# Optimization experiments

Measured on AMD Instinct MI355X. Metric: run time of the kernel, lower is better.

## Reference

```python
import jax, jax.numpy as jnp
import numpy as np

_NUM_RBF = 8
_R_MAX = 3.0  # randn point clouds have radius ~ sqrt(3)
_CENTERS = jnp.linspace(0.0, _R_MAX, _NUM_RBF)
_C15 = float(np.sqrt(15.0))
_C5 = float(np.sqrt(5.0))


def _sph_basis(positions):
    """map_3d_feats_to_basis_functions: 8x0e (radial RBFs) + 1x1o (l=1 SH) + 1x2e (l=2 SH)."""
    centered = positions - jnp.mean(positions, axis=-2, keepdims=True)  # [B,N,3]
    r = jnp.sqrt(jnp.sum(centered * centered, axis=-1) + 1e-12)         # [B,N]
    d = centered / r[..., None]                                         # unit directions
    x, y, z = d[..., 0], d[..., 1], d[..., 2]
    s0 = jnp.exp(-(r[..., None] - _CENTERS) ** 2)                       # [B,N,8] scalar feats (0e)
    sh1 = d                                                             # [B,N,3] (1o)
    sh2 = jnp.stack([_C15 * x * y,
                     _C15 * y * z,
                     0.5 * _C5 * (3.0 * z * z - 1.0),
                     _C15 * x * z,
                     0.5 * _C15 * (x * x - y * y)], axis=-1)            # [B,N,5] (2e)
    return s0, sh1, sh2


def _mix(feat, W):
    # Equivariant per-l channel mixing: feat [B, mul_in, dim_l], W [mul_in, mul_out]
    return jnp.einsum('bci,co->boi', feat, W) / jnp.sqrt(jnp.asarray(W.shape[0], feat.dtype))


def reference(positions, W1a, W1b, W1c, W1d, W2a, W2b, W2c):
    s0, sh1, sh2 = _sph_basis(positions)
    # avg_irreps_with_same_id: average over the N points axis
    s = jnp.mean(s0, axis=-2)[..., None]          # [B,8,1]  8x0e
    v = jnp.mean(sh1, axis=-2)[:, None, :]        # [B,1,3]  1x1o
    # (mean of sh2 is dropped: linear1 output has no 2e)
    # linear1: '8x0e+1x1o+1x2e' -> '6x0e+4x1o' -> '6x0e+4x1o'
    s = _mix(_mix(s, W1a), W1b)                   # [B,6,1]
    v = _mix(_mix(v, W1c), W1d)                   # [B,4,3]
    # linear2: '6x0e+4x1o' -> '6x0e+4x1o' -> '6x0e'
    s = _mix(_mix(s, W2a), W2b)                   # [B,6,1]
    _ = _mix(v, W2c)                              # mid 1o channel, dropped by '6x0e' output
    # torch.cat of the six 0e irreps -> [B,6]
    return s[..., 0]


def setup_inputs() -> dict:
    key = jax.random.key(0)
    ks = jax.random.split(key, 8)
    return {
        'positions': jax.random.normal(ks[0], (32768, 128, 3), dtype=jnp.float32),
        'W1a': jax.random.normal(ks[1], (8, 6), dtype=jnp.float32),
        'W1b': jax.random.normal(ks[2], (6, 6), dtype=jnp.float32),
        'W1c': jax.random.normal(ks[3], (1, 4), dtype=jnp.float32),
        'W1d': jax.random.normal(ks[4], (4, 4), dtype=jnp.float32),
        'W2a': jax.random.normal(ks[5], (6, 6), dtype=jnp.float32),
        'W2b': jax.random.normal(ks[6], (6, 6), dtype=jnp.float32),
        'W2c': jax.random.normal(ks[7], (4, 4), dtype=jnp.float32),
    }
```

## Files before the change

### kernel.cpp

```cpp
#include <hip/hip_runtime.h>


__global__ __launch_bounds__(256) void sph_fused(
    const float* __restrict__ pos,
    const float* __restrict__ W1a, const float* __restrict__ W1b,
    const float* __restrict__ W2a, const float* __restrict__ W2b,
    float* __restrict__ out, int nBatch)
{
    __shared__ float BB[36];
    __shared__ float CC[36];
    __shared__ float MM[64];

    const int t = threadIdx.x;

    if (t < 36) {
        const int c = t / 6, o = t - 6 * c;
        float s = 0.f;
        #pragma unroll
        for (int j = 0; j < 6; ++j) s += W2a[c * 6 + j] * W2b[j * 6 + o];
        BB[t] = s;
    }
    __syncthreads();
    if (t < 36) {
        const int c = t / 6, o = t - 6 * c;
        float s = 0.f;
        #pragma unroll
        for (int j = 0; j < 6; ++j) s += W1b[c * 6 + j] * BB[j * 6 + o];
        CC[t] = s;
    }
    __syncthreads();
    if (t < 64) {
        if (t < 48) {
            const int k = t / 6, o = t - 6 * k;
            float s = 0.f;
            #pragma unroll
            for (int c = 0; c < 6; ++c) s += W1a[k * 6 + c] * CC[c * 6 + o];
            MM[t] = s * (0.024056261216234408f / 128.0f);
        } else {
            MM[t] = 0.f;
        }
    }
    __syncthreads();

    const int lane = t & 63;
    const int wv   = t >> 6;
    const int lsub = lane & 7;
    const int batch = (blockIdx.x * 4 + wv) * 8 + (lane >> 3);
    if (batch >= nBatch) return;

    union { float4 q[12]; float s[48]; } u;
    const float4* p4 = reinterpret_cast<const float4*>(
        pos + (size_t)batch * 384 + lsub * 48);
    #pragma unroll
    for (int j = 0; j < 12; ++j) u.q[j] = p4[j];

    float sx = 0.f, sy = 0.f, sz = 0.f;
    #pragma unroll
    for (int i = 0; i < 16; ++i) {
        sx += u.s[3 * i + 0]; sy += u.s[3 * i + 1]; sz += u.s[3 * i + 2];
    }
    sx += __shfl_xor(sx, 1, 64); sy += __shfl_xor(sy, 1, 64); sz += __shfl_xor(sz, 1, 64);
    sx += __shfl_xor(sx, 2, 64); sy += __shfl_xor(sy, 2, 64); sz += __shfl_xor(sz, 2, 64);
    sx += __shfl_xor(sx, 4, 64); sy += __shfl_xor(sy, 4, 64); sz += __shfl_xor(sz, 4, 64);
    const float mx = sx * (1.f / 128.f), my = sy * (1.f / 128.f), mz = sz * (1.f / 128.f);

    float acc[8] = {0.f, 0.f, 0.f, 0.f, 0.f, 0.f, 0.f, 0.f};
    #pragma unroll
    for (int i = 0; i < 16; ++i) {
        const float dx = u.s[3 * i + 0] - mx;
        const float dy = u.s[3 * i + 1] - my;
        const float dz = u.s[3 * i + 2] - mz;
        const float r = sqrtf(dx * dx + dy * dy + dz * dz + 1e-12f);
        #pragma unroll
        for (int k = 0; k < 8; ++k) {
            const float d = r - (float)k * (3.0f / 7.0f);
            acc[k] += __expf(-(d * d));
        }
    }

    const int l0 = lsub & 1, l1 = (lsub >> 1) & 1, l2 = (lsub >> 2) & 1;
    float bj[4];
    #pragma unroll
    for (int j = 0; j < 4; ++j) {
        const float send = l0 ? acc[2 * j]     : acc[2 * j + 1];
        const float keep = l0 ? acc[2 * j + 1] : acc[2 * j];
        bj[j] = keep + __shfl_xor(send, 1, 64);
    }
    float cj[2];
    #pragma unroll
    for (int j = 0; j < 2; ++j) {
        const float send = l1 ? bj[2 * j]     : bj[2 * j + 1];
        const float keep = l1 ? bj[2 * j + 1] : bj[2 * j];
        cj[j] = keep + __shfl_xor(send, 2, 64);
    }
    float S;
    {
        const float send = l2 ? cj[0] : cj[1];
        const float keep = l2 ? cj[1] : cj[0];
        S = keep + __shfl_xor(send, 4, 64);
    }

    const int laneBase = lane & 56;
    float oacc = 0.f;
    #pragma unroll
    for (int k = 0; k < 8; ++k) {
        const float sk = __shfl(S, laneBase + k, 64);
        oacc += sk * MM[k * 6 + lsub];
    }
    if (lsub < 6) out[batch * 6 + lsub] = oacc;
}

extern "C" void kernel_launch(void* const* d_in, const int* in_sizes, int n_in,
                              void* d_out, int out_size, void* d_ws, size_t ws_size,
                              hipStream_t stream) {
    const float* pos = (const float*)d_in[0];
    const float* W1a = (const float*)d_in[1];
    const float* W1b = (const float*)d_in[2];
    const float* W2a = (const float*)d_in[5];
    const float* W2b = (const float*)d_in[6];
    float* out = (float*)d_out;

    const int nBatch = in_sizes[0] / 384;
    const int batchesPerBlock = 32;
    const int grid = (nBatch + batchesPerBlock - 1) / batchesPerBlock;

    sph_fused<<<dim3(grid), dim3(256), 0, stream>>>(pos, W1a, W1b, W2a, W2b, out, nBatch);
}
```

Before: 18.23 us.

## Stage coalesced loads through LDS, use 16 lanes per batch, factor RBF exponentials

Each wave now loads positions as fully coalesced float4 chunks and transposes them through a swizzled LDS staging buffer, so every lane handles 8 points and a 16-lane group covers one batch. The eight RBF exponentials per point are replaced by two exps plus a running product with precomputed constant weights. Output stores are gathered into 24 contiguous lanes, and each block now covers 16 batches instead of 32. This adds 24KB of LDS per block, which may limit occupancy. The stage writes and reads happen without a barrier, relying only on an lgkmcnt wait within the wave.

```diff
diff --git a/kernel.cpp b/kernel.cpp
--- a/kernel.cpp
+++ b/kernel.cpp
@@ -10,6 +10,7 @@
     __shared__ float BB[36];
     __shared__ float CC[36];
     __shared__ float MM[64];
+    __shared__ float4 stage[4][384];
 
     const int t = threadIdx.x;
 
@@ -42,42 +43,69 @@
     }
     __syncthreads();
 
+    const int w    = t >> 6;
     const int lane = t & 63;
-    const int wv   = t >> 6;
-    const int lsub = lane & 7;
-    const int batch = (blockIdx.x * 4 + wv) * 8 + (lane >> 3);
-    if (batch >= nBatch) return;
+    const int wave = blockIdx.x * 4 + w;
+    const int wbatch = wave * 4;
+    if (wbatch >= nBatch) return;
 
-    union { float4 q[12]; float s[48]; } u;
-    const float4* p4 = reinterpret_cast<const float4*>(
-        pos + (size_t)batch * 384 + lsub * 48);
+    const int nChunks = nBatch * 96;
+    const int wchunk  = wave * 384;
+    const float4* p4 = reinterpret_cast<const float4*>(pos);
     #pragma unroll
-    for (int j = 0; j < 12; ++j) u.q[j] = p4[j];
+    for (int j = 0; j < 6; ++j) {
+        const int q = j * 64 + lane;
+        int gc = wchunk + q;
+        if (gc >= nChunks) gc = nChunks - 1;
+        const float4 v = p4[gc];
+        const int o = (q * 171) >> 10;
+        const int s = q - 6 * o;
+        stage[w][s * 64 + (o ^ s)] = v;
+    }
+    asm volatile("s_waitcnt lgkmcnt(0)" ::: "memory");
+
+    union { float4 q4[6]; float f[24]; } u;
+    #pragma unroll
+    for (int s = 0; s < 6; ++s) u.q4[s] = stage[w][s * 64 + (lane ^ s)];
 
     float sx = 0.f, sy = 0.f, sz = 0.f;
     #pragma unroll
-    for (int i = 0; i < 16; ++i) {
-        sx += u.s[3 * i + 0]; sy += u.s[3 * i + 1]; sz += u.s[3 * i + 2];
+    for (int i = 0; i < 8; ++i) {
+        sx += u.f[3 * i + 0]; sy += u.f[3 * i + 1]; sz += u.f[3 * i + 2];
     }
-    sx += __shfl_xor(sx, 1, 64); sy += __shfl_xor(sy, 1, 64); sz += __shfl_xor(sz, 1, 64);
-    sx += __shfl_xor(sx, 2, 64); sy += __shfl_xor(sy, 2, 64); sz += __shfl_xor(sz, 2, 64);
-    sx += __shfl_xor(sx, 4, 64); sy += __shfl_xor(sy, 4, 64); sz += __shfl_xor(sz, 4, 64);
+    #pragma unroll
+    for (int m = 1; m <= 8; m <<= 1) {
+        sx += __shfl_xor(sx, m, 64);
+        sy += __shfl_xor(sy, m, 64);
+        sz += __shfl_xor(sz, m, 64);
+    }
     const float mx = sx * (1.f / 128.f), my = sy * (1.f / 128.f), mz = sz * (1.f / 128.f);
 
+    const float WK1 = 0.83220583f, WK2 = 0.47965235f, WK3 = 0.19146295f,
+                WK4 = 0.05293049f, WK5 = 0.01013418f, WK6 = 0.00134381f,
+                WK7 = 1.2340980e-4f;
     float acc[8] = {0.f, 0.f, 0.f, 0.f, 0.f, 0.f, 0.f, 0.f};
     #pragma unroll
-    for (int i = 0; i < 16; ++i) {
-        const float dx = u.s[3 * i + 0] - mx;
-        const float dy = u.s[3 * i + 1] - my;
-        const float dz = u.s[3 * i + 2] - mz;
-        const float r = sqrtf(dx * dx + dy * dy + dz * dz + 1e-12f);
-        #pragma unroll
-        for (int k = 0; k < 8; ++k) {
-            const float d = r - (float)k * (3.0f / 7.0f);
-            acc[k] += __expf(-(d * d));
-        }
+    for (int i = 0; i < 8; ++i) {
+        const float dx = u.f[3 * i + 0] - mx;
+        const float dy = u.f[3 * i + 1] - my;
+        const float dz = u.f[3 * i + 2] - mz;
+        const float r2 = fmaf(dx, dx, fmaf(dy, dy, fmaf(dz, dz, 1e-12f)));
+        const float r  = sqrtf(r2);
+        const float E0 = __expf(-r2);
+        const float Bf = __expf(r * (6.0f / 7.0f));
+        float p = E0;
+        acc[0] += E0;
+        p *= Bf; acc[1] = fmaf(p, WK1, acc[1]);
+        p *= Bf; acc[2] = fmaf(p, WK2, acc[2]);
+        p *= Bf; acc[3] = fmaf(p, WK3, acc[3]);
+        p *= Bf; acc[4] = fmaf(p, WK4, acc[4]);
+        p *= Bf; acc[5] = fmaf(p, WK5, acc[5]);
+        p *= Bf; acc[6] = fmaf(p, WK6, acc[6]);
+        p *= Bf; acc[7] = fmaf(p, WK7, acc[7]);
     }
 
+    const int lsub = lane & 15;
     const int l0 = lsub & 1, l1 = (lsub >> 1) & 1, l2 = (lsub >> 2) & 1;
     float bj[4];
     #pragma unroll
@@ -99,15 +127,18 @@
         const float keep = l2 ? cj[1] : cj[0];
         S = keep + __shfl_xor(send, 4, 64);
     }
+    S += __shfl_xor(S, 8, 64);
 
-    const int laneBase = lane & 56;
+    const int gb = lane & 48;
     float oacc = 0.f;
     #pragma unroll
-    for (int k = 0; k < 8; ++k) {
-        const float sk = __shfl(S, laneBase + k, 64);
-        oacc += sk * MM[k * 6 + lsub];
-    }
-    if (lsub < 6) out[batch * 6 + lsub] = oacc;
+    for (int k = 0; k < 8; ++k)
+        oacc = fmaf(__shfl(S, gb + k, 64), MM[k * 6 + lsub], oacc);
+
+    const int LL = (lane < 24) ? lane : 0;
+    const int g = LL / 6, r = LL - 6 * g;
+    const float val = __shfl(oacc, g * 16 + r, 64);
+    if (lane < 24 && (wbatch + g) < nBatch) out[wbatch * 6 + lane] = val;
 }
 
 extern "C" void kernel_launch(void* const* d_in, const int* in_sizes, int n_in,
@@ -121,7 +152,7 @@
     float* out = (float*)d_out;
 
     const int nBatch = in_sizes[0] / 384;
-    const int batchesPerBlock = 32;
+    const int batchesPerBlock = 16;
     const int grid = (nBatch + batchesPerBlock - 1) / batchesPerBlock;
 
     sph_fused<<<dim3(grid), dim3(256), 0, stream>>>(pos, W1a, W1b, W2a, W2b, out, nBatch);
```

New measurement: 17.42 us. 4.4% less time.

## Persistent double-buffered waves with DPP reductions and factored RBF exponentials

Applied to the files above, without the earlier changes.

Changes the kernel to a persistent grid capped at 1024 blocks, where each wave processes 4 batches per tile with 16 lanes per batch and software double-buffers the next tile's loads while computing the current one. Shuffle-based reductions become DPP row-rotate reductions across 16 lanes. The eight per-point RBF exponentials are replaced by two exps and a running product with precomputed weights, using exp(-(r-c_k)^2) = exp(-r^2)·exp(2rc_k)·exp(-c_k^2). This reduces transcendental work and hides memory latency, but the running-product factorisation may lose accuracy for large r.

```diff
diff --git a/kernel.cpp b/kernel.cpp
--- a/kernel.cpp
+++ b/kernel.cpp
@@ -1,15 +1,28 @@
 #include <hip/hip_runtime.h>
 
 
-__global__ __launch_bounds__(256) void sph_fused(
+template <int N>
+__device__ __forceinline__ float ror16(float v) {
+    return __int_as_float(__builtin_amdgcn_update_dpp(
+        0, __float_as_int(v), 0x120 | N, 0xF, 0xF, true));
+}
+__device__ __forceinline__ float rowsum16(float v) {
+    v += ror16<1>(v);
+    v += ror16<2>(v);
+    v += ror16<4>(v);
+    v += ror16<8>(v);
+    return v;
+}
+
+__global__ __launch_bounds__(256, 4) void sph_fused(
     const float* __restrict__ pos,
     const float* __restrict__ W1a, const float* __restrict__ W1b,
     const float* __restrict__ W2a, const float* __restrict__ W2b,
     float* __restrict__ out, int nBatch)
 {
-    __shared__ float BB[36];
-    __shared__ float CC[36];
-    __shared__ float MM[64];
+    __shared__ float BBs[36];
+    __shared__ float CCs[36];
+    __shared__ float MMs[48];
 
     const int t = threadIdx.x;
 
@@ -18,96 +31,126 @@
         float s = 0.f;
         #pragma unroll
         for (int j = 0; j < 6; ++j) s += W2a[c * 6 + j] * W2b[j * 6 + o];
-        BB[t] = s;
+        BBs[t] = s;
     }
     __syncthreads();
     if (t < 36) {
         const int c = t / 6, o = t - 6 * c;
         float s = 0.f;
         #pragma unroll
-        for (int j = 0; j < 6; ++j) s += W1b[c * 6 + j] * BB[j * 6 + o];
-        CC[t] = s;
+        for (int j = 0; j < 6; ++j) s += W1b[c * 6 + j] * BBs[j * 6 + o];
+        CCs[t] = s;
     }
     __syncthreads();
-    if (t < 64) {
-        if (t < 48) {
-            const int k = t / 6, o = t - 6 * k;
-            float s = 0.f;
-            #pragma unroll
-            for (int c = 0; c < 6; ++c) s += W1a[k * 6 + c] * CC[c * 6 + o];
-            MM[t] = s * (0.024056261216234408f / 128.0f);
-        } else {
-            MM[t] = 0.f;
-        }
+    if (t < 48) {
+        const int k = t / 6, o = t - 6 * k;
+        float s = 0.f;
+        #pragma unroll
+        for (int c = 0; c < 6; ++c) s += W1a[k * 6 + c] * CCs[c * 6 + o];
+        MMs[t] = s * (0.024056261216234408f / 128.0f);
     }
     __syncthreads();
 
     const int lane = t & 63;
-    const int wv   = t >> 6;
-    const int lsub = lane & 7;
-    const int batch = (blockIdx.x * 4 + wv) * 8 + (lane >> 3);
-    if (batch >= nBatch) return;
+    const int w    = t >> 6;
+    const int lsub = lane & 15;
+    const int grp  = lane >> 4;
 
-    union { float4 q[12]; float s[48]; } u;
-    const float4* p4 = reinterpret_cast<const float4*>(
-        pos + (size_t)batch * 384 + lsub * 48);
+    const int col = (lsub < 6) ? lsub : 0;
+    float Mcol[8];
     #pragma unroll
-    for (int j = 0; j < 12; ++j) u.q[j] = p4[j];
+    for (int k = 0; k < 8; ++k) Mcol[k] = MMs[k * 6 + col];
 
-    float sx = 0.f, sy = 0.f, sz = 0.f;
-    #pragma unroll
-    for (int i = 0; i < 16; ++i) {
-        sx += u.s[3 * i + 0]; sy += u.s[3 * i + 1]; sz += u.s[3 * i + 2];
+    const int nTiles = (nBatch + 3) >> 2;
+    const int nWaves = gridDim.x * 4;
+    int tile = blockIdx.x * 4 + w;
+    if (tile >= nTiles) return;
+
+    const float4* __restrict__ p4 = reinterpret_cast<const float4*>(pos);
+    const int maxC = nBatch * 96 - 6;
+
+    union Pts { float4 q[6]; float f[24]; };
+    Pts A, B;
+
+    const float WK1 = 0.83220583f, WK2 = 0.47965235f, WK3 = 0.19146295f,
+                WK4 = 0.05293049f, WK5 = 0.01013418f, WK6 = 0.00134381f,
+                WK7 = 1.2340980e-4f;
+
+#define LOADT(U, T) do {                                                   \
+    int base_ = (T) * 384 + grp * 96 + lsub * 6;                           \
+    if (base_ > maxC) base_ = maxC;    \
+    _Pragma("unroll")                                                      \
+    for (int j_ = 0; j_ < 6; ++j_) (U).q[j_] = p4[base_ + j_];             \
+} while (0)
+
+#define COMPUTE(U, T) do {                                                 \
+    float sx_ = 0.f, sy_ = 0.f, sz_ = 0.f;                                 \
+    _Pragma("unroll")                                                      \
+    for (int i_ = 0; i_ < 8; ++i_) {                                       \
+        sx_ += (U).f[3 * i_ + 0];                                          \
+        sy_ += (U).f[3 * i_ + 1];                                          \
+        sz_ += (U).f[3 * i_ + 2];                                          \
+    }                                                                      \
+    sx_ = rowsum16(sx_); sy_ = rowsum16(sy_); sz_ = rowsum16(sz_);         \
+    const float mx_ = sx_ * (1.f / 128.f);                                 \
+    const float my_ = sy_ * (1.f / 128.f);                                 \
+    const float mz_ = sz_ * (1.f / 128.f);                                 \
+    float a0_=0.f,a1_=0.f,a2_=0.f,a3_=0.f,a4_=0.f,a5_=0.f,a6_=0.f,a7_=0.f; \
+    _Pragma("unroll")                                                      \
+    for (int i_ = 0; i_ < 8; ++i_) {                                       \
+        const float dx_ = (U).f[3 * i_ + 0] - mx_;                         \
+        const float dy_ = (U).f[3 * i_ + 1] - my_;                         \
+        const float dz_ = (U).f[3 * i_ + 2] - mz_;                         \
+        const float r2_ = fmaf(dx_, dx_, fmaf(dy_, dy_, fmaf(dz_, dz_, 1e-12f))); \
+        float r_;                                                          \
+        asm("v_sqrt_f32 %0, %1" : "=v"(r_) : "v"(r2_));                    \
+        const float E0_ = __expf(-r2_);                                    \
+        const float Bf_ = __expf(r_ * (6.0f / 7.0f));                      \
+        float p_ = E0_;                                                    \
+        a0_ += E0_;                                                        \
+        p_ *= Bf_; a1_ = fmaf(p_, WK1, a1_);                               \
+        p_ *= Bf_; a2_ = fmaf(p_, WK2, a2_);                               \
+        p_ *= Bf_; a3_ = fmaf(p_, WK3, a3_);                               \
+        p_ *= Bf_; a4_ = fmaf(p_, WK4, a4_);                               \
+        p_ *= Bf_; a5_ = fmaf(p_, WK5, a5_);                               \
+        p_ *= Bf_; a6_ = fmaf(p_, WK6, a6_);                               \
+        p_ *= Bf_; a7_ = fmaf(p_, WK7, a7_);                               \
+    }                                                                      \
+    a0_ = rowsum16(a0_); a1_ = rowsum16(a1_);                              \
+    a2_ = rowsum16(a2_); a3_ = rowsum16(a3_);                              \
+    a4_ = rowsum16(a4_); a5_ = rowsum16(a5_);                              \
+    a6_ = rowsum16(a6_); a7_ = rowsum16(a7_);                              \
+    float o_ = a0_ * Mcol[0];                                              \
+    o_ = fmaf(a1_, Mcol[1], o_); o_ = fmaf(a2_, Mcol[2], o_);              \
+    o_ = fmaf(a3_, Mcol[3], o_); o_ = fmaf(a4_, Mcol[4], o_);              \
+    o_ = fmaf(a5_, Mcol[5], o_); o_ = fmaf(a6_, Mcol[6], o_);              \
+    o_ = fmaf(a7_, Mcol[7], o_);                                           \
+    const int batch_ = (T) * 4 + grp;                                      \
+    if (lsub < 6 && batch_ < nBatch) out[batch_ * 6 + lsub] = o_;          \
+} while (0)
+
+    LOADT(A, tile);
+    for (;;) {
+        int tn = tile + nWaves;
+        if (tn < nTiles) {
+            LOADT(B, tn);
+            COMPUTE(A, tile);
+        } else {
+            COMPUTE(A, tile);
+            break;
+        }
+        tile = tn; tn = tile + nWaves;
+        if (tn < nTiles) {
+            LOADT(A, tn);
+            COMPUTE(B, tile);
+        } else {
+            COMPUTE(B, tile);
+            break;
+        }
+        tile = tn;
     }
-    sx += __shfl_xor(sx, 1, 64); sy += __shfl_xor(sy, 1, 64); sz += __shfl_xor(sz, 1, 64);
-    sx += __shfl_xor(sx, 2, 64); sy += __shfl_xor(sy, 2, 64); sz += __shfl_xor(sz, 2, 64);
-    sx += __shfl_xor(sx, 4, 64); sy += __shfl_xor(sy, 4, 64); sz += __shfl_xor(sz, 4, 64);
-    const float mx = sx * (1.f / 128.f), my = sy * (1.f / 128.f), mz = sz * (1.f / 128.f);
-
-    float acc[8] = {0.f, 0.f, 0.f, 0.f, 0.f, 0.f, 0.f, 0.f};
-    #pragma unroll
-    for (int i = 0; i < 16; ++i) {
-        const float dx = u.s[3 * i + 0] - mx;
-        const float dy = u.s[3 * i + 1] - my;
-        const float dz = u.s[3 * i + 2] - mz;
-        const float r = sqrtf(dx * dx + dy * dy + dz * dz + 1e-12f);
-        #pragma unroll
-        for (int k = 0; k < 8; ++k) {
-            const float d = r - (float)k * (3.0f / 7.0f);
-            acc[k] += __expf(-(d * d));
-        }
-    }
-
-    const int l0 = lsub & 1, l1 = (lsub >> 1) & 1, l2 = (lsub >> 2) & 1;
-    float bj[4];
-    #pragma unroll
-    for (int j = 0; j < 4; ++j) {
-        const float send = l0 ? acc[2 * j]     : acc[2 * j + 1];
-        const float keep = l0 ? acc[2 * j + 1] : acc[2 * j];
-        bj[j] = keep + __shfl_xor(send, 1, 64);
-    }
-    float cj[2];
-    #pragma unroll
-    for (int j = 0; j < 2; ++j) {
-        const float send = l1 ? bj[2 * j]     : bj[2 * j + 1];
-        const float keep = l1 ? bj[2 * j + 1] : bj[2 * j];
-        cj[j] = keep + __shfl_xor(send, 2, 64);
-    }
-    float S;
-    {
-        const float send = l2 ? cj[0] : cj[1];
-        const float keep = l2 ? cj[1] : cj[0];
-        S = keep + __shfl_xor(send, 4, 64);
-    }
-
-    const int laneBase = lane & 56;
-    float oacc = 0.f;
-    #pragma unroll
-    for (int k = 0; k < 8; ++k) {
-        const float sk = __shfl(S, laneBase + k, 64);
-        oacc += sk * MM[k * 6 + lsub];
-    }
-    if (lsub < 6) out[batch * 6 + lsub] = oacc;
+#undef LOADT
+#undef COMPUTE
 }
 
 extern "C" void kernel_launch(void* const* d_in, const int* in_sizes, int n_in,
@@ -121,8 +164,9 @@
     float* out = (float*)d_out;
 
     const int nBatch = in_sizes[0] / 384;
-    const int batchesPerBlock = 32;
-    const int grid = (nBatch + batchesPerBlock - 1) / batchesPerBlock;
+    const int nTiles = (nBatch + 3) / 4;
+    int grid = (nTiles + 3) / 4;
+    if (grid > 1024) grid = 1024;
 
     sph_fused<<<dim3(grid), dim3(256), 0, stream>>>(pos, W1a, W1b, W2a, W2b, out, nBatch);
 }
```

Result: faster. 15.55 us (-14.7%).
